# Performance work log

Hardware: AMD Instinct MI355X
Metric: run time of the kernel (lower is better)

The kernel has to match this reference:

```python
import jax, jax.numpy as jnp
import numpy as np

SEQ = 4096
BLOCK = 64
NUM_RAND = 3
B, H, D = 1, 12, 64


def _build_bigbird_mask(seq_len=SEQ, block=BLOCK, num_rand=NUM_RAND, seed=0):
    """Dense [S,S] BigBird mask: global first/last block, window +-1 block,
    num_rand random blocks per middle row (mirrors bigbird_block_rand_mask)."""
    nb = seq_len // block
    rng = np.random.RandomState(seed)
    m = np.zeros((nb, nb), dtype=np.int32)
    # global blocks (first & last block attend/are attended everywhere)
    m[0, :] = 1
    m[-1, :] = 1
    m[:, 0] = 1
    m[:, -1] = 1
    # sliding window of one block on each side
    idx = np.arange(nb)
    win = np.abs(idx[:, None] - idx[None, :]) <= 1
    m[win] = 1
    # random blocks for middle rows, excluding window and global columns
    for i in range(1, nb - 1):
        cand = np.array([j for j in range(1, nb - 1) if abs(j - i) > 1], dtype=np.int32)
        sel = rng.permutation(cand)[:num_rand]
        m[i, sel] = 1
    return np.kron(m, np.ones((block, block), dtype=np.int32))


def setup_inputs() -> dict:
    key = jax.random.key(0)
    kq, kk, kv = jax.random.split(key, 3)
    q = jax.random.normal(kq, (B, H, SEQ, D), dtype=jnp.float32)
    k = jax.random.normal(kk, (B, H, SEQ, D), dtype=jnp.float32)
    v = jax.random.normal(kv, (B, H, SEQ, D), dtype=jnp.float32)
    mask = jnp.asarray(_build_bigbird_mask(), dtype=jnp.int32)  # [S, S]
    return {"q": q, "k": k, "v": v, "mask": mask}


def reference(q, k, v, mask):
    # OriginalFullAttention with dense BigBird mask:
    # scores = QK^T / sqrt(D); masked positions get -10000 additive bias.
    scale = 1.0 / np.sqrt(D).astype(np.float32)
    scores = jnp.einsum("bhqd,bhkd->bhqk", q, k) * scale
    adder = (1.0 - mask.astype(scores.dtype)) * jnp.asarray(-10000.0, scores.dtype)
    probs = jax.nn.softmax(scores + adder[None, None, :, :], axis=-1)
    out = jnp.einsum("bhqk,bhkd->bhqd", probs, v)  # [B, H, S, D]
    return out
```

## Files before the change

kernel.cpp:

```cpp
#include <hip/hip_runtime.h>
#include <stdint.h>

#define SEQ 4096
#define DH  64
#define NB  64
#define NH  12

typedef float  f32x4  __attribute__((ext_vector_type(4)));
typedef short  s16x8  __attribute__((ext_vector_type(8)));
typedef unsigned short ushort_t;
typedef unsigned long long u64;

__device__ __forceinline__ unsigned short f2bf(float x){
    union { float f; unsigned u; } c; c.f = x;
    unsigned u = c.u;
    u += 0x7fffu + ((u >> 16) & 1u);
    return (unsigned short)(u >> 16);
}

__device__ __forceinline__ s16x8 pack8(f32x4 a, f32x4 b){
    s16x8 r;
#pragma unroll
    for (int i = 0; i < 4; ++i) { r[i] = (short)f2bf(a[i]); r[i+4] = (short)f2bf(b[i]); }
    return r;
}

__device__ __forceinline__ int swz(int row, int col){
    return row * 64 + (col ^ ((row & 7) << 3));
}

#define GLOAD_LDS(gp, lp) __builtin_amdgcn_global_load_lds( \
    (const __attribute__((address_space(1))) unsigned int*)(gp), \
    (__attribute__((address_space(3))) unsigned int*)(lp), 16, 0, 0)

#define KBF_OFF   0
#define VTB_OFF   6291456
#define PART_OFF  12582912
#define BMP_OFF   15777792
#define WS_NEED   15778304
#define SLOT_F    4160

__global__ __launch_bounds__(256) void bb_conv(
        const float* __restrict__ k, const float* __restrict__ v,
        const int* __restrict__ mask,
        ushort_t* __restrict__ kbf, ushort_t* __restrict__ vtb,
        u64* __restrict__ bmp)
{
    const int kb = blockIdx.x, h = blockIdx.y;
    const int tid = threadIdx.x;
    __shared__ float vls[64*65];

    if (h == 0 && tid < 64){
        bool a = mask[(size_t)(kb*64)*SEQ + tid*64] != 0;
        u64 bm = __ballot(a);
        if (tid == 0) bmp[kb] = bm;
    }

    const int j = tid >> 2, c = (tid & 3) * 16;
    const size_t gsrc = (size_t)h*SEQ*DH + (size_t)(kb*64 + j)*DH + c;
    const size_t tdst = ((size_t)h*NB + kb) * 4096;

    {
        f32x4 a0 = *(const f32x4*)(k + gsrc);
        f32x4 a1 = *(const f32x4*)(k + gsrc + 4);
        f32x4 a2 = *(const f32x4*)(k + gsrc + 8);
        f32x4 a3 = *(const f32x4*)(k + gsrc + 12);
        *(s16x8*)&kbf[tdst + swz(j, c    )] = pack8(a0, a1);
        *(s16x8*)&kbf[tdst + swz(j, c + 8)] = pack8(a2, a3);
    }
    {
        f32x4 b0 = *(const f32x4*)(v + gsrc);
        f32x4 b1 = *(const f32x4*)(v + gsrc + 4);
        f32x4 b2 = *(const f32x4*)(v + gsrc + 8);
        f32x4 b3 = *(const f32x4*)(v + gsrc + 12);
#pragma unroll
        for (int i = 0; i < 4; ++i){
            vls[j*65 + c + i     ] = b0[i];
            vls[j*65 + c + 4 + i ] = b1[i];
            vls[j*65 + c + 8 + i ] = b2[i];
            vls[j*65 + c + 12 + i] = b3[i];
        }
    }
    __syncthreads();
    {
        const int d = tid >> 2, jc = (tid & 3) * 16;
        s16x8 r0, r1;
#pragma unroll
        for (int i = 0; i < 8; ++i){
            r0[i] = (short)f2bf(vls[(jc + i    )*65 + d]);
            r1[i] = (short)f2bf(vls[(jc + i + 8)*65 + d]);
        }
        *(s16x8*)&vtb[tdst + swz(d, jc    )] = r0;
        *(s16x8*)&vtb[tdst + swz(d, jc + 8)] = r1;
    }
}

__global__ __launch_bounds__(256) void bb_main(
        const float* __restrict__ q,
        const ushort_t* __restrict__ kbf, const ushort_t* __restrict__ vtb,
        const u64* __restrict__ bmp,
        float* __restrict__ out, float* __restrict__ part)
{
    const int lin = blockIdx.x;
    const int job = (lin & 7) * 117 + (lin >> 3);
    const int h   = job / 78;
    const int x   = job - h * 78;

    int qb, wq = -1, sp = 0; u64 rmask;
    if (x < 62) { qb = x + 1; rmask = ~0ull; }
    else { int e = x - 62; wq = e >> 3; sp = e & 7; qb = wq ? 63 : 0; rmask = 0xFFull << (sp*8); }

    const int tid  = threadIdx.x;
    const int wave = tid >> 6;
    const int lane = tid & 63;
    const int lrow = lane & 15;
    const int lgrp = lane >> 4;

    __shared__ __align__(16) ushort_t KV[2][2][4096];
    __shared__ __align__(16) ushort_t Pw[4][16*64];

    const size_t hoff = (size_t)h * SEQ * DH;

    s16x8 qf[2];
    {
        const float* qp = q + hoff + (size_t)(qb*64 + wave*16 + lrow) * DH + lgrp*8;
#pragma unroll
        for (int kc = 0; kc < 2; ++kc){
            f32x4 a = *(const f32x4*)(qp + kc*32);
            f32x4 b = *(const f32x4*)(qp + kc*32 + 4);
            a *= 0.125f; b *= 0.125f;
            qf[kc] = pack8(a, b);
        }
    }

    u64 bits = bmp[qb] & rmask;

    const ushort_t* Kb = kbf + (size_t)h * (NB*4096);
    const ushort_t* Vb = vtb + (size_t)h * (NB*4096);

    const f32x4 zero = {0.f,0.f,0.f,0.f};
    f32x4 oa[4] = {zero, zero, zero, zero};
    float lp[4] = {0.f,0.f,0.f,0.f};

    const int soff = wave*1024 + lane*16;
#define STAGE(gbase, lbase)                                          \
    {                                                                \
        const char* g0 = (const char*)(gbase) + soff;                \
        char*       l0 = (char*)(lbase) + wave*1024;                 \
        GLOAD_LDS(g0, l0);                                           \
        GLOAD_LDS(g0 + 4096, l0 + 4096);                             \
    }

    if (bits){
        int kb = __builtin_ctzll(bits); bits &= bits - 1;
        STAGE(Kb + (size_t)kb*4096, &KV[0][0][0]);
        STAGE(Vb + (size_t)kb*4096, &KV[0][1][0]);
        __syncthreads();
        int cur = 0;
        for (;;){
            const bool more = (bits != 0);
            if (more){
                int nkb = __builtin_ctzll(bits); bits &= bits - 1;
                STAGE(Kb + (size_t)nkb*4096, &KV[cur^1][0][0]);
                STAGE(Vb + (size_t)nkb*4096, &KV[cur^1][1][0]);
            }

            const ushort_t* Kt = &KV[cur][0][0];
            const ushort_t* Vt = &KV[cur][1][0];
            s16x8 kf[8];
#pragma unroll
            for (int jt = 0; jt < 4; ++jt)
#pragma unroll
                for (int kc = 0; kc < 2; ++kc)
                    kf[jt*2+kc] = *(const s16x8*)&Kt[swz(jt*16+lrow, kc*32 + lgrp*8)];

            f32x4 sa[4] = {zero, zero, zero, zero};
#pragma unroll
            for (int jt = 0; jt < 4; ++jt)
#pragma unroll
                for (int kc = 0; kc < 2; ++kc)
                    sa[jt] = __builtin_amdgcn_mfma_f32_16x16x32_bf16(qf[kc], kf[jt*2+kc], sa[jt], 0, 0, 0);

            s16x8 vf[8];
#pragma unroll
            for (int dc = 0; dc < 4; ++dc)
#pragma unroll
                for (int hh = 0; hh < 2; ++hh)
                    vf[dc*2+hh] = *(const s16x8*)&Vt[swz(dc*16+lrow, hh*32 + lgrp*8)];

#pragma unroll
            for (int jt = 0; jt < 4; ++jt)
#pragma unroll
                for (int r = 0; r < 4; ++r){
                    float p = __expf(sa[jt][r]);
                    sa[jt][r] = p;
                    lp[r] += p;
                }
#pragma unroll
            for (int jt = 0; jt < 4; ++jt)
#pragma unroll
                for (int r = 0; r < 4; ++r)
                    Pw[wave][swz(lgrp*4 + r, jt*16 + lrow)] = f2bf(sa[jt][r]);

            s16x8 pf0 = *(const s16x8*)&Pw[wave][swz(lrow,      lgrp*8)];
            s16x8 pf1 = *(const s16x8*)&Pw[wave][swz(lrow, 32 + lgrp*8)];
#pragma unroll
            for (int dc = 0; dc < 4; ++dc){
                oa[dc] = __builtin_amdgcn_mfma_f32_16x16x32_bf16(pf0, vf[dc*2  ], oa[dc], 0, 0, 0);
                oa[dc] = __builtin_amdgcn_mfma_f32_16x16x32_bf16(pf1, vf[dc*2+1], oa[dc], 0, 0, 0);
            }

            if (!more) break;
            __syncthreads();
            cur ^= 1;
        }
    }
#undef STAGE

#pragma unroll
    for (int r = 0; r < 4; ++r){
        float t = lp[r];
        t += __shfl_xor(t, 1);
        t += __shfl_xor(t, 2);
        t += __shfl_xor(t, 4);
        t += __shfl_xor(t, 8);
        lp[r] = t;
    }

    if (wq < 0){
        float inv[4];
#pragma unroll
        for (int r = 0; r < 4; ++r) inv[r] = lp[r] > 0.f ? 1.0f / lp[r] : 0.f;
        float* op = out + hoff + (size_t)(qb*64 + wave*16) * DH;
#pragma unroll
        for (int dc = 0; dc < 4; ++dc)
#pragma unroll
            for (int r = 0; r < 4; ++r)
                op[(size_t)(lgrp*4 + r)*DH + dc*16 + lrow] = oa[dc][r] * inv[r];
    } else {
        float* pp = part + ((size_t)(h*2 + wq)*8 + sp) * SLOT_F;
#pragma unroll
        for (int dc = 0; dc < 4; ++dc)
#pragma unroll
            for (int r = 0; r < 4; ++r)
                pp[(size_t)(wave*16 + lgrp*4 + r)*DH + dc*16 + lrow] = oa[dc][r];
        if (lrow == 0){
#pragma unroll
            for (int r = 0; r < 4; ++r)
                pp[4096 + wave*16 + lgrp*4 + r] = lp[r];
        }
    }
}

__global__ __launch_bounds__(256) void bb_comb(
        const float* __restrict__ part, float* __restrict__ out)
{
    const int h = blockIdx.x >> 1, wq = blockIdx.x & 1;
    const int qb = wq ? 63 : 0;
    const int tid = threadIdx.x;
    const int i = tid >> 2, cg = (tid & 3) * 16;

    const float* base = part + (size_t)(h*2 + wq) * 8 * SLOT_F;
    f32x4 acc[4] = {{0,0,0,0},{0,0,0,0},{0,0,0,0},{0,0,0,0}};
    float ls = 0.f;
#pragma unroll
    for (int s = 0; s < 8; ++s){
        const float* p = base + (size_t)s * SLOT_F;
#pragma unroll
        for (int c4 = 0; c4 < 4; ++c4)
            acc[c4] += *(const f32x4*)(p + (size_t)i*DH + cg + c4*4);
        ls += p[4096 + i];
    }
    const float inv = ls > 0.f ? 1.0f / ls : 0.f;
    float* op = out + (size_t)h*SEQ*DH + (size_t)(qb*64 + i)*DH + cg;
#pragma unroll
    for (int c4 = 0; c4 < 4; ++c4){
        f32x4 r = acc[c4] * inv;
        *(f32x4*)(op + c4*4) = r;
    }
}

__global__ __launch_bounds__(256) void bb_attn_fb(
        const float* __restrict__ q, const float* __restrict__ k,
        const float* __restrict__ v, const int* __restrict__ mask,
        float* __restrict__ out)
{
    const int qb   = blockIdx.x;
    const int h    = blockIdx.y;
    const int tid  = threadIdx.x;
    const int wave = tid >> 6;
    const int lane = tid & 63;
    const int lrow = lane & 15;
    const int lgrp = lane >> 4;

    __shared__ __align__(16) ushort_t Kb[64*64];
    __shared__ __align__(16) ushort_t Vt[64*64];
    __shared__ __align__(16) ushort_t Pw[4][16*64];

    const size_t hoff = (size_t)h * SEQ * DH;
    const int qrow = qb*64 + wave*16 + lrow;
    const float* qp = q + hoff + (size_t)qrow * DH + lgrp*8;
    s16x8 qf[2];
#pragma unroll
    for (int kc = 0; kc < 2; ++kc){
        f32x4 a = *(const f32x4*)(qp + kc*32);
        f32x4 b = *(const f32x4*)(qp + kc*32 + 4);
        a *= 0.125f; b *= 0.125f;
        qf[kc] = pack8(a, b);
    }
    const f32x4 zero = {0.f,0.f,0.f,0.f};
    f32x4 oa[4] = {zero, zero, zero, zero};
    float m_run[4] = {-1e30f,-1e30f,-1e30f,-1e30f};
    float l_run[4] = {0.f,0.f,0.f,0.f};
    const int* mrow = mask + (size_t)(qb*64) * SEQ;
    const int kr  = tid >> 2, kcg  = tid & 3;
    const int j2  = tid >> 3, dgrp = tid & 7;

    for (int kb = 0; kb < NB; ++kb){
        if (mrow[kb*64] == 0) continue;
        __syncthreads();
        {
            const float* kp = k + hoff + (size_t)(kb*64 + kr) * DH + kcg*16;
            f32x4 a0 = *(const f32x4*)(kp);
            f32x4 a1 = *(const f32x4*)(kp+4);
            f32x4 a2 = *(const f32x4*)(kp+8);
            f32x4 a3 = *(const f32x4*)(kp+12);
            *(s16x8*)&Kb[swz(kr, kcg*16    )] = pack8(a0, a1);
            *(s16x8*)&Kb[swz(kr, kcg*16 + 8)] = pack8(a2, a3);
        }
        {
            const float* vp0 = v + hoff + (size_t)(kb*64 + 2*j2) * DH + dgrp*8;
            f32x4 b0 = *(const f32x4*)(vp0);
            f32x4 b1 = *(const f32x4*)(vp0+4);
            f32x4 b2 = *(const f32x4*)(vp0+DH);
            f32x4 b3 = *(const f32x4*)(vp0+DH+4);
            float r0[8] = {b0[0],b0[1],b0[2],b0[3],b1[0],b1[1],b1[2],b1[3]};
            float r1[8] = {b2[0],b2[1],b2[2],b2[3],b3[0],b3[1],b3[2],b3[3]};
#pragma unroll
            for (int i = 0; i < 8; ++i){
                int dd = (i + dgrp) & 7;
                int d  = dgrp*8 + dd;
                unsigned val = (unsigned)f2bf(r0[dd]) | ((unsigned)f2bf(r1[dd]) << 16);
                *(unsigned*)&Vt[swz(d, 2*j2)] = val;
            }
        }
        __syncthreads();
        f32x4 sa[4] = {zero, zero, zero, zero};
#pragma unroll
        for (int jt = 0; jt < 4; ++jt)
#pragma unroll
            for (int kc = 0; kc < 2; ++kc){
                s16x8 kf = *(const s16x8*)&Kb[swz(jt*16 + lrow, kc*32 + lgrp*8)];
                sa[jt] = __builtin_amdgcn_mfma_f32_16x16x32_bf16(qf[kc], kf, sa[jt], 0, 0, 0);
            }
        float fac[4];
#pragma unroll
        for (int r = 0; r < 4; ++r){
            float mx = fmaxf(fmaxf(sa[0][r], sa[1][r]), fmaxf(sa[2][r], sa[3][r]));
            mx = fmaxf(mx, __shfl_xor(mx, 1));
            mx = fmaxf(mx, __shfl_xor(mx, 2));
            mx = fmaxf(mx, __shfl_xor(mx, 4));
            mx = fmaxf(mx, __shfl_xor(mx, 8));
            float mn = fmaxf(m_run[r], mx);
            fac[r] = __expf(m_run[r] - mn);
            m_run[r] = mn;
        }
#pragma unroll
        for (int r = 0; r < 4; ++r){
            float p0 = __expf(sa[0][r] - m_run[r]);
            float p1 = __expf(sa[1][r] - m_run[r]);
            float p2 = __expf(sa[2][r] - m_run[r]);
            float p3 = __expf(sa[3][r] - m_run[r]);
            sa[0][r]=p0; sa[1][r]=p1; sa[2][r]=p2; sa[3][r]=p3;
            float sm = p0+p1+p2+p3;
            sm += __shfl_xor(sm, 1);
            sm += __shfl_xor(sm, 2);
            sm += __shfl_xor(sm, 4);
            sm += __shfl_xor(sm, 8);
            l_run[r] = l_run[r]*fac[r] + sm;
        }
#pragma unroll
        for (int dc = 0; dc < 4; ++dc)
#pragma unroll
            for (int r = 0; r < 4; ++r) oa[dc][r] *= fac[r];
#pragma unroll
        for (int jt = 0; jt < 4; ++jt)
#pragma unroll
            for (int r = 0; r < 4; ++r)
                Pw[wave][swz(lgrp*4 + r, jt*16 + lrow)] = f2bf(sa[jt][r]);
        s16x8 pf0 = *(const s16x8*)&Pw[wave][swz(lrow,      lgrp*8)];
        s16x8 pf1 = *(const s16x8*)&Pw[wave][swz(lrow, 32 + lgrp*8)];
#pragma unroll
        for (int dc = 0; dc < 4; ++dc){
            s16x8 v0 = *(const s16x8*)&Vt[swz(dc*16 + lrow,      lgrp*8)];
            s16x8 v1 = *(const s16x8*)&Vt[swz(dc*16 + lrow, 32 + lgrp*8)];
            oa[dc] = __builtin_amdgcn_mfma_f32_16x16x32_bf16(pf0, v0, oa[dc], 0, 0, 0);
            oa[dc] = __builtin_amdgcn_mfma_f32_16x16x32_bf16(pf1, v1, oa[dc], 0, 0, 0);
        }
    }
    float inv[4];
#pragma unroll
    for (int r = 0; r < 4; ++r) inv[r] = 1.0f / l_run[r];
    float* op = out + hoff + (size_t)(qb*64 + wave*16) * DH;
#pragma unroll
    for (int dc = 0; dc < 4; ++dc)
#pragma unroll
        for (int r = 0; r < 4; ++r)
            op[(size_t)(lgrp*4 + r) * DH + dc*16 + lrow] = oa[dc][r] * inv[r];
}

extern "C" void kernel_launch(void* const* d_in, const int* in_sizes, int n_in,
                              void* d_out, int out_size, void* d_ws, size_t ws_size,
                              hipStream_t stream)
{
    const float* q    = (const float*)d_in[0];
    const float* k    = (const float*)d_in[1];
    const float* v    = (const float*)d_in[2];
    const int*   mask = (const int*)d_in[3];
    float* out = (float*)d_out;

    if (ws_size < (size_t)WS_NEED){
        dim3 grid(NB, NH, 1);
        bb_attn_fb<<<grid, 256, 0, stream>>>(q, k, v, mask, out);
        return;
    }

    char* ws = (char*)d_ws;
    ushort_t* kbf = (ushort_t*)(ws + KBF_OFF);
    ushort_t* vtb = (ushort_t*)(ws + VTB_OFF);
    float*    prt = (float*)   (ws + PART_OFF);
    u64*      bmp = (u64*)     (ws + BMP_OFF);

    bb_conv<<<dim3(NB, NH, 1), 256, 0, stream>>>(k, v, mask, kbf, vtb, bmp);
    bb_main<<<dim3(936, 1, 1), 256, 0, stream>>>(q, kbf, vtb, bmp, out, prt);
    bb_comb<<<dim3(24, 1, 1), 256, 0, stream>>>(prt, out);
}
```

Baseline: 41.58 us.

## Use 32x32x16 MFMA with register P transpose and split-K wave reduction

The main sparse-attention kernel switches from 16x16x32 MFMA tiles to 32x32x16 tiles. Each wave now handles 32 query rows and half of the key block, computing S transposed (K as the A operand) so the probabilities can be repacked for the PV MFMA with v_permlane32_swap in registers, with no round trip through the per-wave P buffer in LDS. Partial outputs and row sums from the two key-half waves are combined through shared memory at the end. This removes LDS traffic and a serialising LDS store/load per key block, at the cost of an extra epilogue reduction and more accumulator registers. The other kernel only inlines the swizzle helper.

```diff
diff --git a/kernel.cpp b/kernel.cpp
--- a/kernel.cpp
+++ b/kernel.cpp
@@ -6,8 +6,9 @@
 #define NB  64
 #define NH  12
 
-typedef float  f32x4  __attribute__((ext_vector_type(4)));
-typedef short  s16x8  __attribute__((ext_vector_type(8)));
+typedef float  f32x4   __attribute__((ext_vector_type(4)));
+typedef float  f32x16  __attribute__((ext_vector_type(16)));
+typedef short  s16x8   __attribute__((ext_vector_type(8)));
 typedef unsigned short ushort_t;
 typedef unsigned long long u64;
 
@@ -16,6 +17,10 @@
     unsigned u = c.u;
     u += 0x7fffu + ((u >> 16) & 1u);
     return (unsigned short)(u >> 16);
+}
+
+__device__ __forceinline__ unsigned pk2(float lo, float hi){
+    return (unsigned)f2bf(lo) | ((unsigned)f2bf(hi) << 16);
 }
 
 __device__ __forceinline__ s16x8 pack8(f32x4 a, f32x4 b){
@@ -113,23 +118,25 @@
     const int tid  = threadIdx.x;
     const int wave = tid >> 6;
     const int lane = tid & 63;
-    const int lrow = lane & 15;
-    const int lgrp = lane >> 4;
+    const int l31  = lane & 31;
+    const int hi   = lane >> 5;
+    const int qh   = wave >> 1;
+    const int kh   = wave & 1;
 
     __shared__ __align__(16) ushort_t KV[2][2][4096];
-    __shared__ __align__(16) ushort_t Pw[4][16*64];
+    __shared__ float lsm[64];
 
     const size_t hoff = (size_t)h * SEQ * DH;
 
-    s16x8 qf[2];
+    s16x8 qf[4];
     {
-        const float* qp = q + hoff + (size_t)(qb*64 + wave*16 + lrow) * DH + lgrp*8;
-#pragma unroll
-        for (int kc = 0; kc < 2; ++kc){
-            f32x4 a = *(const f32x4*)(qp + kc*32);
-            f32x4 b = *(const f32x4*)(qp + kc*32 + 4);
+        const float* qp = q + hoff + (size_t)(qb*64 + qh*32 + l31) * DH + 8*hi;
+#pragma unroll
+        for (int c = 0; c < 4; ++c){
+            f32x4 a = *(const f32x4*)(qp + c*16);
+            f32x4 b = *(const f32x4*)(qp + c*16 + 4);
             a *= 0.125f; b *= 0.125f;
-            qf[kc] = pack8(a, b);
+            qf[c] = pack8(a, b);
         }
     }
 
@@ -138,9 +145,8 @@
     const ushort_t* Kb = kbf + (size_t)h * (NB*4096);
     const ushort_t* Vb = vtb + (size_t)h * (NB*4096);
 
-    const f32x4 zero = {0.f,0.f,0.f,0.f};
-    f32x4 oa[4] = {zero, zero, zero, zero};
-    float lp[4] = {0.f,0.f,0.f,0.f};
+    f32x16 oa0 = {0.f}, oa1 = {0.f};
+    float lp = 0.f;
 
     const int soff = wave*1024 + lane*16;
 #define STAGE(gbase, lbase)                                          \
@@ -167,47 +173,41 @@
 
             const ushort_t* Kt = &KV[cur][0][0];
             const ushort_t* Vt = &KV[cur][1][0];
-            s16x8 kf[8];
-#pragma unroll
-            for (int jt = 0; jt < 4; ++jt)
-#pragma unroll
-                for (int kc = 0; kc < 2; ++kc)
-                    kf[jt*2+kc] = *(const s16x8*)&Kt[swz(jt*16+lrow, kc*32 + lgrp*8)];
-
-            f32x4 sa[4] = {zero, zero, zero, zero};
-#pragma unroll
-            for (int jt = 0; jt < 4; ++jt)
-#pragma unroll
-                for (int kc = 0; kc < 2; ++kc)
-                    sa[jt] = __builtin_amdgcn_mfma_f32_16x16x32_bf16(qf[kc], kf[jt*2+kc], sa[jt], 0, 0, 0);
-
-            s16x8 vf[8];
-#pragma unroll
-            for (int dc = 0; dc < 4; ++dc)
-#pragma unroll
-                for (int hh = 0; hh < 2; ++hh)
-                    vf[dc*2+hh] = *(const s16x8*)&Vt[swz(dc*16+lrow, hh*32 + lgrp*8)];
-
-#pragma unroll
-            for (int jt = 0; jt < 4; ++jt)
-#pragma unroll
-                for (int r = 0; r < 4; ++r){
-                    float p = __expf(sa[jt][r]);
-                    sa[jt][r] = p;
-                    lp[r] += p;
-                }
-#pragma unroll
-            for (int jt = 0; jt < 4; ++jt)
-#pragma unroll
-                for (int r = 0; r < 4; ++r)
-                    Pw[wave][swz(lgrp*4 + r, jt*16 + lrow)] = f2bf(sa[jt][r]);
-
-            s16x8 pf0 = *(const s16x8*)&Pw[wave][swz(lrow,      lgrp*8)];
-            s16x8 pf1 = *(const s16x8*)&Pw[wave][swz(lrow, 32 + lgrp*8)];
-#pragma unroll
-            for (int dc = 0; dc < 4; ++dc){
-                oa[dc] = __builtin_amdgcn_mfma_f32_16x16x32_bf16(pf0, vf[dc*2  ], oa[dc], 0, 0, 0);
-                oa[dc] = __builtin_amdgcn_mfma_f32_16x16x32_bf16(pf1, vf[dc*2+1], oa[dc], 0, 0, 0);
+
+            f32x16 sa = {0.f};
+#pragma unroll
+            for (int c = 0; c < 4; ++c){
+                s16x8 kf = *(const s16x8*)&Kt[swz(kh*32 + l31, c*16 + 8*hi)];
+                sa = __builtin_amdgcn_mfma_f32_32x32x16_bf16(kf, qf[c], sa, 0, 0, 0);
+            }
+
+            float p[16];
+#pragma unroll
+            for (int r = 0; r < 16; ++r){
+                p[r] = __expf(sa[r]);
+                lp += p[r];
+            }
+
+            s16x8 pa[2];
+#pragma unroll
+            for (int s = 0; s < 2; ++s){
+                unsigned a1 = pk2(p[8*s+0], p[8*s+1]);
+                unsigned b1 = pk2(p[8*s+4], p[8*s+5]);
+                unsigned a2 = pk2(p[8*s+2], p[8*s+3]);
+                unsigned b2 = pk2(p[8*s+6], p[8*s+7]);
+                asm("v_permlane32_swap_b32 %0, %1" : "+v"(a1), "+v"(b1));
+                asm("v_permlane32_swap_b32 %0, %1" : "+v"(a2), "+v"(b2));
+                union { unsigned w[4]; s16x8 v; } u;
+                u.w[0] = a1; u.w[1] = a2; u.w[2] = b1; u.w[3] = b2;
+                pa[s] = u.v;
+            }
+
+#pragma unroll
+            for (int s = 0; s < 2; ++s){
+                s16x8 v0 = *(const s16x8*)&Vt[swz(     l31, kh*32 + s*16 + 8*hi)];
+                s16x8 v1 = *(const s16x8*)&Vt[swz(32 + l31, kh*32 + s*16 + 8*hi)];
+                oa0 = __builtin_amdgcn_mfma_f32_32x32x16_bf16(pa[s], v0, oa0, 0, 0, 0);
+                oa1 = __builtin_amdgcn_mfma_f32_32x32x16_bf16(pa[s], v1, oa1, 0, 0, 0);
             }
 
             if (!more) break;
@@ -217,37 +217,43 @@
     }
 #undef STAGE
 
-#pragma unroll
-    for (int r = 0; r < 4; ++r){
-        float t = lp[r];
-        t += __shfl_xor(t, 1);
-        t += __shfl_xor(t, 2);
-        t += __shfl_xor(t, 4);
-        t += __shfl_xor(t, 8);
-        lp[r] = t;
-    }
-
-    if (wq < 0){
-        float inv[4];
-#pragma unroll
-        for (int r = 0; r < 4; ++r) inv[r] = lp[r] > 0.f ? 1.0f / lp[r] : 0.f;
-        float* op = out + hoff + (size_t)(qb*64 + wave*16) * DH;
-#pragma unroll
-        for (int dc = 0; dc < 4; ++dc)
-#pragma unroll
-            for (int r = 0; r < 4; ++r)
-                op[(size_t)(lgrp*4 + r)*DH + dc*16 + lrow] = oa[dc][r] * inv[r];
-    } else {
-        float* pp = part + ((size_t)(h*2 + wq)*8 + sp) * SLOT_F;
-#pragma unroll
-        for (int dc = 0; dc < 4; ++dc)
-#pragma unroll
-            for (int r = 0; r < 4; ++r)
-                pp[(size_t)(wave*16 + lgrp*4 + r)*DH + dc*16 + lrow] = oa[dc][r];
-        if (lrow == 0){
-#pragma unroll
-            for (int r = 0; r < 4; ++r)
-                pp[4096 + wave*16 + lgrp*4 + r] = lp[r];
+    float lpf = lp + __shfl_xor(lp, 32);
+
+    __syncthreads();
+    float* msm = (float*)&KV[0][0][0];
+
+    if (kh == 1){
+#pragma unroll
+        for (int r = 0; r < 16; ++r){
+            const int cr = (r&3) + 8*(r>>2) + 4*hi;
+            msm[(qh*32 + cr)*64 +      l31] = oa0[r];
+            msm[(qh*32 + cr)*64 + 32 + l31] = oa1[r];
+        }
+        if (lane < 32) lsm[qh*32 + lane] = lpf;
+    }
+    __syncthreads();
+
+    if (kh == 0){
+        const float lt = lpf + lsm[qh*32 + l31];
+        if (wq < 0){
+            const float inv = lt > 0.f ? 1.0f / lt : 0.f;
+            float* op = out + hoff + (size_t)(qb*64 + qh*32) * DH;
+#pragma unroll
+            for (int r = 0; r < 16; ++r){
+                const int cr = (r&3) + 8*(r>>2) + 4*hi;
+                const float ir = __shfl(inv, cr);
+                op[(size_t)cr*DH +      l31] = (oa0[r] + msm[(qh*32 + cr)*64 +      l31]) * ir;
+                op[(size_t)cr*DH + 32 + l31] = (oa1[r] + msm[(qh*32 + cr)*64 + 32 + l31]) * ir;
+            }
+        } else {
+            float* pp = part + ((size_t)(h*2 + wq)*8 + sp) * SLOT_F;
+#pragma unroll
+            for (int r = 0; r < 16; ++r){
+                const int cr = (r&3) + 8*(r>>2) + 4*hi;
+                pp[(qh*32 + cr)*64 +      l31] = oa0[r] + msm[(qh*32 + cr)*64 +      l31];
+                pp[(qh*32 + cr)*64 + 32 + l31] = oa1[r] + msm[(qh*32 + cr)*64 + 32 + l31];
+            }
+            if (lane < 32) pp[4096 + qh*32 + lane] = lt;
         }
     }
 }
@@ -325,8 +331,8 @@
             f32x4 a1 = *(const f32x4*)(kp+4);
             f32x4 a2 = *(const f32x4*)(kp+8);
             f32x4 a3 = *(const f32x4*)(kp+12);
-            *(s16x8*)&Kb[swz(kr, kcg*16    )] = pack8(a0, a1);
-            *(s16x8*)&Kb[swz(kr, kcg*16 + 8)] = pack8(a2, a3);
+            *(s16x8*)&Kb[(kr*64) + (kcg*16     ^ ((kr&7)<<3))] = pack8(a0, a1);
+            *(s16x8*)&Kb[(kr*64) + ((kcg*16+8) ^ ((kr&7)<<3))] = pack8(a2, a3);
         }
         {
             const float* vp0 = v + hoff + (size_t)(kb*64 + 2*j2) * DH + dgrp*8;
@@ -341,7 +347,7 @@
                 int dd = (i + dgrp) & 7;
                 int d  = dgrp*8 + dd;
                 unsigned val = (unsigned)f2bf(r0[dd]) | ((unsigned)f2bf(r1[dd]) << 16);
-                *(unsigned*)&Vt[swz(d, 2*j2)] = val;
+                *(unsigned*)&Vt[(d*64) + (2*j2 ^ ((d&7)<<3))] = val;
             }
         }
         __syncthreads();
@@ -350,7 +356,8 @@
         for (int jt = 0; jt < 4; ++jt)
 #pragma unroll
             for (int kc = 0; kc < 2; ++kc){
-                s16x8 kf = *(const s16x8*)&Kb[swz(jt*16 + lrow, kc*32 + lgrp*8)];
+                int row = jt*16 + lrow, col = kc*32 + lgrp*8;
+                s16x8 kf = *(const s16x8*)&Kb[row*64 + (col ^ ((row&7)<<3))];
                 sa[jt] = __builtin_amdgcn_mfma_f32_16x16x32_bf16(qf[kc], kf, sa[jt], 0, 0, 0);
             }
         float fac[4];
@@ -386,14 +393,17 @@
 #pragma unroll
         for (int jt = 0; jt < 4; ++jt)
 #pragma unroll
-            for (int r = 0; r < 4; ++r)
-                Pw[wave][swz(lgrp*4 + r, jt*16 + lrow)] = f2bf(sa[jt][r]);
-        s16x8 pf0 = *(const s16x8*)&Pw[wave][swz(lrow,      lgrp*8)];
-        s16x8 pf1 = *(const s16x8*)&Pw[wave][swz(lrow, 32 + lgrp*8)];
+            for (int r = 0; r < 4; ++r){
+                int row = lgrp*4 + r, col = jt*16 + lrow;
+                Pw[wave][row*64 + (col ^ ((row&7)<<3))] = f2bf(sa[jt][r]);
+            }
+        s16x8 pf0 = *(const s16x8*)&Pw[wave][lrow*64 + ((     lgrp*8) ^ ((lrow&7)<<3))];
+        s16x8 pf1 = *(const s16x8*)&Pw[wave][lrow*64 + ((32 + lgrp*8) ^ ((lrow&7)<<3))];
 #pragma unroll
         for (int dc = 0; dc < 4; ++dc){
-            s16x8 v0 = *(const s16x8*)&Vt[swz(dc*16 + lrow,      lgrp*8)];
-            s16x8 v1 = *(const s16x8*)&Vt[swz(dc*16 + lrow, 32 + lgrp*8)];
+            int row0 = dc*16 + lrow;
+            s16x8 v0 = *(const s16x8*)&Vt[row0*64 + ((     lgrp*8) ^ ((row0&7)<<3))];
+            s16x8 v1 = *(const s16x8*)&Vt[row0*64 + ((32 + lgrp*8) ^ ((row0&7)<<3))];
             oa[dc] = __builtin_amdgcn_mfma_f32_16x16x32_bf16(pf0, v0, oa[dc], 0, 0, 0);
             oa[dc] = __builtin_amdgcn_mfma_f32_16x16x32_bf16(pf1, v1, oa[dc], 0, 0, 0);
         }
```

New measurement: 42.46 us. 1.02x slower.
